# Kernel optimization log

Measured on AMD Instinct MI355X. Metric: run time of the kernel, lower is better.

## Reference

```python
import jax, jax.numpy as jnp
import numpy as np

NUM_HEADS = 16
EMB = 1024
HEAD = 64
SEQ = 2048
BATCH = 4


def setup_inputs() -> dict:
    key = jax.random.key(0)
    ks = jax.random.split(key, 6)
    s = EMB ** -0.5
    x = jax.random.normal(ks[0], (BATCH, SEQ, EMB), dtype=jnp.float32)
    # per-head projection weights stacked: [H, E, D] (Linear(emb, head, bias=False) per head)
    Wq = jax.random.normal(ks[1], (NUM_HEADS, EMB, HEAD), dtype=jnp.float32) * s
    Wk = jax.random.normal(ks[2], (NUM_HEADS, EMB, HEAD), dtype=jnp.float32) * s
    Wv = jax.random.normal(ks[3], (NUM_HEADS, EMB, HEAD), dtype=jnp.float32) * s
    # output projection Linear(head*num_heads, emb): weight [E, H*D], bias [E]
    Wo = jax.random.normal(ks[4], (EMB, NUM_HEADS * HEAD), dtype=jnp.float32) * ((NUM_HEADS * HEAD) ** -0.5)
    bo = jax.random.normal(ks[5], (EMB,), dtype=jnp.float32) * 0.01
    return {"x": x, "Wq": Wq, "Wk": Wk, "Wv": Wv, "Wo": Wo, "bo": bo}


def reference(x, Wq, Wk, Wv, Wo, bo):
    B, S, E = x.shape
    scale = HEAD ** -0.5
    # batched per-head projections: [B, H, S, D]
    q = jnp.einsum('bse,hed->bhsd', x, Wq)
    k = jnp.einsum('bse,hed->bhsd', x, Wk)
    v = jnp.einsum('bse,hed->bhsd', x, Wv)
    scores = jnp.einsum('bhqd,bhkd->bhqk', q, k) * scale
    causal = jnp.tril(jnp.ones((S, S), dtype=bool))
    scores = jnp.where(causal, scores, jnp.finfo(scores.dtype).min)
    attn = jax.nn.softmax(scores, axis=-1)  # dropout disabled (eval/deterministic)
    ctx = jnp.einsum('bhqk,bhkd->bhqd', attn, v)
    # concat heads along last dim (head-major order, matching torch.cat)
    concat = ctx.transpose(0, 2, 1, 3).reshape(B, S, NUM_HEADS * HEAD)
    out = concat @ Wo.T + bo
    return out
```

## Files before the change

kernel.cpp:

```cpp
#include <hip/hip_runtime.h>

#define NHEADS 16
#define EMB 1024
#define HDIM 64
#define SEQ 2048
#define BATCH 4

typedef unsigned short u16;
typedef __attribute__((ext_vector_type(8))) __bf16 bf16x8;
typedef __attribute__((ext_vector_type(4))) float f32x4;

#if __has_builtin(__builtin_amdgcn_exp2f)
#define EXP2(x) __builtin_amdgcn_exp2f(x)
#else
#define EXP2(x) __expf((x)*0.69314718056f)
#endif
#define CL2E 0.18033688011112042f

#define BARRIER() __builtin_amdgcn_s_barrier()
#define SB0() __builtin_amdgcn_sched_barrier(0)
#define PRIO1() __builtin_amdgcn_s_setprio(1)
#define PRIO0() __builtin_amdgcn_s_setprio(0)
#define VMCNT(n) asm volatile("s_waitcnt vmcnt(" #n ")" ::: "memory")

__device__ __forceinline__ u16 f2bf(float f) {
  union { float f; unsigned u; } v; v.f = f;
  unsigned r = v.u + 0x7fffu + ((v.u >> 16) & 1u);
  return (u16)(r >> 16);
}
__device__ __forceinline__ unsigned pk2bf(float a, float b) {
  union { __bf16 h[2]; unsigned u; } x;
  x.h[0] = (__bf16)a; x.h[1] = (__bf16)b; return x.u;
}
__device__ __forceinline__ void gl16(const void* g, void* l) {
  __builtin_amdgcn_global_load_lds(
      (const __attribute__((address_space(1))) unsigned*)g,
      (__attribute__((address_space(3))) unsigned*)l, 16, 0, 0);
}
__device__ __forceinline__ unsigned PKLO(unsigned a, unsigned b) {
  return __builtin_amdgcn_perm(a, b, 0x01000504u);
}
__device__ __forceinline__ unsigned PKHI(unsigned a, unsigned b) {
  return __builtin_amdgcn_perm(a, b, 0x03020706u);
}

__global__ __launch_bounds__(256) void k_cvt(const float* __restrict__ in,
                                             u16* __restrict__ out, int n4) {
  int i = blockIdx.x * 256 + threadIdx.x;
  if (i >= n4) return;
  f32x4 v = *(const f32x4*)(in + (size_t)i * 4);
  uint2 o;
  o.x = (unsigned)f2bf(v[0]) | ((unsigned)f2bf(v[1]) << 16);
  o.y = (unsigned)f2bf(v[2]) | ((unsigned)f2bf(v[3]) << 16);
  *(uint2*)(out + (size_t)i * 4) = o;
}

__global__ __launch_bounds__(256) void k_packw(const float* __restrict__ Wq,
                                               const float* __restrict__ Wk,
                                               const float* __restrict__ Wv,
                                               u16* __restrict__ Wt) {
  const int mh = blockIdx.x;
  const int e0 = blockIdx.y * 64;
  const int mtx = mh >> 4, h = mh & 15;
  const float* W = (mtx == 0 ? Wq : (mtx == 1 ? Wk : Wv)) + (size_t)h * EMB * HDIM;
  __shared__ u16 sT[64][65];
  const int t = threadIdx.x;
  {
    int e = t >> 2, d0 = (t & 3) * 16;
#pragma unroll
    for (int jj = 0; jj < 4; jj++) {
      f32x4 v = *(const f32x4*)(W + (size_t)(e0 + e) * HDIM + d0 + jj * 4);
#pragma unroll
      for (int kk = 0; kk < 4; kk++) sT[e][d0 + jj * 4 + kk] = f2bf(v[kk]);
    }
  }
  __syncthreads();
  {
    int d = t >> 2, eb = (t & 3) * 16;
#pragma unroll
    for (int j = 0; j < 16; j++)
      Wt[(size_t)(mh * 64 + d) * EMB + e0 + eb + j] = sT[eb + j][d];
  }
}

__global__ __launch_bounds__(512, 2) void k_gemm_qkv8(const u16* __restrict__ Xb,
                                                      const u16* __restrict__ Wt,
                                                      u16* __restrict__ Q,
                                                      u16* __restrict__ K,
                                                      u16* __restrict__ V) {
  extern __shared__ __align__(16) char smem[];
  const int bid = blockIdx.x;
  const int l = (bid & 7) * 64 + (bid >> 3);
  const int mt = l & 31, nt = l >> 5;
  const int m0 = mt * 256, n0 = nt * 192;

  const int t = threadIdx.x;
  const int wave = t >> 6, lane = t & 63, lr = lane & 15, lg = lane >> 4;
  const int wr = (wave >> 2) * 128;
  const int wc = (wave & 3) * 48;

  const f32x4 fz = {0.f, 0.f, 0.f, 0.f};
  f32x4 acc[8][3];
#pragma unroll
  for (int i = 0; i < 8; i++)
#pragma unroll
    for (int j = 0; j < 3; j++) acc[i][j] = fz;

  bf16x8 af[4][2], bfr[3][2];

  auto SROUND = [&](char* ldsbase, int rbase, const u16* src, int gRowBase, int kt) {
    int rs = rbase + wave * 8;
    int row = rs + (lane >> 3);
    int gc = (lane & 7) ^ (row & 7);
    gl16(src + (size_t)(gRowBase + row) * EMB + kt * 64 + gc * 8, ldsbase + rs * 128);
  };
  auto LOADA = [&](const char* bA, int mh) {
#pragma unroll
    for (int mf = 0; mf < 4; mf++)
#pragma unroll
      for (int kf = 0; kf < 2; kf++) {
        int row = wr + mh * 64 + mf * 16 + lr;
        af[mf][kf] = *(const bf16x8*)(bA + row * 128 + ((kf * 64 + lg * 16) ^ ((row & 7) << 4)));
      }
  };
  auto LOADB = [&](const char* bB) {
#pragma unroll
    for (int nf = 0; nf < 3; nf++)
#pragma unroll
      for (int kf = 0; kf < 2; kf++) {
        int row = wc + nf * 16 + lr;
        bfr[nf][kf] = *(const bf16x8*)(bB + row * 128 + ((kf * 64 + lg * 16) ^ ((row & 7) << 4)));
      }
  };

#define MFMAPH(MH)                                                                         \
  do {                                                                                     \
    _Pragma("unroll") for (int kf = 0; kf < 2; kf++)                                       \
    _Pragma("unroll") for (int mf = 0; mf < 4; mf++)                                       \
    _Pragma("unroll") for (int nf = 0; nf < 3; nf++)                                       \
      acc[(MH)*4 + mf][nf] = __builtin_amdgcn_mfma_f32_16x16x32_bf16(                      \
          af[mf][kf], bfr[nf][kf], acc[(MH)*4 + mf][nf], 0, 0, 0);                         \
  } while (0)

  const int NT = EMB / 64;
  {
    char* nA = smem;
    char* nB = smem + 32768;
    SROUND(nB, 0, Wt, n0, 0); SROUND(nB, 64, Wt, n0, 0); SROUND(nB, 128, Wt, n0, 0);
    SROUND(nA, 0, Xb, m0, 0);
    SROUND(nA, 64, Xb, m0, 0); SROUND(nA, 128, Xb, m0, 0); SROUND(nA, 192, Xb, m0, 0);
  }
  VMCNT(0);
  BARRIER();

  for (int tt = 0; tt < NT - 1; tt++) {
    const int cb = tt & 1, nb = cb ^ 1;
    char* bA = smem + cb * 57344;
    char* bB = bA + 32768;
    char* nA = smem + nb * 57344;
    char* nB = nA + 32768;
    SROUND(nB, 0, Wt, n0, tt + 1);
    SROUND(nB, 64, Wt, n0, tt + 1);
    SROUND(nB, 128, Wt, n0, tt + 1);
    SROUND(nA, 0, Xb, m0, tt + 1);
    VMCNT(5);
    BARRIER(); SB0();
    LOADA(bA, 0);
    LOADB(bB);
    PRIO1(); MFMAPH(0); PRIO0();
    BARRIER();
    SROUND(nA, 64, Xb, m0, tt + 1);
    SROUND(nA, 128, Xb, m0, tt + 1);
    SROUND(nA, 192, Xb, m0, tt + 1);
    VMCNT(7);
    BARRIER(); SB0();
    LOADA(bA, 1);
    PRIO1(); MFMAPH(1); PRIO0();
    BARRIER();
  }
  {
    char* bA = smem + ((NT - 1) & 1) * 57344;
    char* bB = bA + 32768;
    VMCNT(0);
    BARRIER(); SB0();
    LOADA(bA, 0);
    LOADB(bB);
    PRIO1(); MFMAPH(0); PRIO0();
    LOADA(bA, 1);
    PRIO1(); MFMAPH(1); PRIO0();
  }
#undef MFMAPH

  const int b = m0 >> 11;
  const int s0 = m0 & 2047;
#pragma unroll
  for (int am = 0; am < 8; am++)
#pragma unroll
    for (int nf = 0; nf < 3; nf++)
#pragma unroll
      for (int r = 0; r < 4; r++) {
        int row = wr + am * 16 + lg * 4 + r;
        int n = n0 + wc + nf * 16 + lr;
        int mtx = n >> 10, h = (n >> 6) & 15, d = n & 63;
        u16* dst = (mtx == 0 ? Q : (mtx == 1 ? K : V));
        dst[((size_t)(b * NHEADS + h) * SEQ + s0 + row) * HDIM + d] = f2bf(acc[am][nf][r]);
      }
}

__global__ __launch_bounds__(256, 3) void k_attn(const u16* __restrict__ Q,
                                                 const u16* __restrict__ K,
                                                 const u16* __restrict__ V,
                                                 u16* __restrict__ Cc) {
  const int bh = blockIdx.x;
  const int qt = 15 - (int)blockIdx.y;
  const int b = bh >> 4, h = bh & 15;
  const int t = threadIdx.x;
  const int wq = t >> 6, lane = t & 63, lr = lane & 15, lg = lane >> 4;
  const size_t base = (size_t)bh * SEQ * HDIM;

  __shared__ __align__(16) char sK[64 * 128];
  __shared__ __align__(16) char sV[64 * 128];
  __shared__ __align__(16) char sP[128 * 128];

#pragma unroll
  for (int i = 0; i < 4; i++) {
    int rb = wq * 32 + i * 8;
    int row = rb + (lane >> 3);
    int gc = (lane & 7) ^ (row & 7);
    gl16(Q + base + (size_t)(qt * 128 + row) * HDIM + gc * 8, sP + rb * 128);
  }
  __syncthreads();
  bf16x8 qf[2][2];
#pragma unroll
  for (int q2 = 0; q2 < 2; q2++)
#pragma unroll
    for (int kf = 0; kf < 2; kf++) {
      int row = wq * 32 + q2 * 16 + lr;
      qf[q2][kf] = *(const bf16x8*)(sP + row * 128 + ((kf * 64 + lg * 16) ^ ((row & 7) << 4)));
    }

  const f32x4 fz = {0.f, 0.f, 0.f, 0.f};
  f32x4 ot[4][2];
#pragma unroll
  for (int df = 0; df < 4; df++)
#pragma unroll
    for (int q2 = 0; q2 < 2; q2++) ot[df][q2] = fz;
  float m_[2] = {-1e30f, -1e30f}, l_[2] = {0.f, 0.f};

  const int nsteps = 2 * qt + 2;
  for (int step = 0; step < nsteps; step++) {
    const int k0 = step * 64;
    __syncthreads();
#pragma unroll
    for (int i = 0; i < 2; i++) {
      int rb = wq * 16 + i * 8;
      int row = rb + (lane >> 3);
      int gc = (lane & 7) ^ (row & 7);
      gl16(K + base + (size_t)(k0 + row) * HDIM + gc * 8, sK + rb * 128);
    }
    {
      const int kvb = (t & 15) * 4, db = (t >> 4) * 4;
      const u16* vp = V + base + (size_t)(k0 + kvb) * HDIM + db;
      uint2 v0 = *(const uint2*)(vp);
      uint2 v1 = *(const uint2*)(vp + HDIM);
      uint2 v2 = *(const uint2*)(vp + 2 * HDIM);
      uint2 v3 = *(const uint2*)(vp + 3 * HDIM);
      uint2 w0 = {PKLO(v0.x, v1.x), PKLO(v2.x, v3.x)};
      uint2 w1 = {PKHI(v0.x, v1.x), PKHI(v2.x, v3.x)};
      uint2 w2 = {PKLO(v0.y, v1.y), PKLO(v2.y, v3.y)};
      uint2 w3 = {PKHI(v0.y, v1.y), PKHI(v2.y, v3.y)};
      *(uint2*)(sV + (db + 0) * 128 + ((kvb * 2) ^ (((db + 0) & 7) << 4))) = w0;
      *(uint2*)(sV + (db + 1) * 128 + ((kvb * 2) ^ (((db + 1) & 7) << 4))) = w1;
      *(uint2*)(sV + (db + 2) * 128 + ((kvb * 2) ^ (((db + 2) & 7) << 4))) = w2;
      *(uint2*)(sV + (db + 3) * 128 + ((kvb * 2) ^ (((db + 3) & 7) << 4))) = w3;
    }
    __syncthreads();

    f32x4 st[4][2];
#pragma unroll
    for (int kvf = 0; kvf < 4; kvf++)
#pragma unroll
      for (int q2 = 0; q2 < 2; q2++) st[kvf][q2] = fz;
#pragma unroll
    for (int kf = 0; kf < 2; kf++) {
      bf16x8 kfr[4];
#pragma unroll
      for (int kvf = 0; kvf < 4; kvf++) {
        int row = kvf * 16 + lr;
        kfr[kvf] = *(const bf16x8*)(sK + row * 128 + ((kf * 64 + lg * 16) ^ ((row & 7) << 4)));
      }
#pragma unroll
      for (int kvf = 0; kvf < 4; kvf++)
#pragma unroll
        for (int q2 = 0; q2 < 2; q2++)
          st[kvf][q2] = __builtin_amdgcn_mfma_f32_16x16x32_bf16(kfr[kvf], qf[q2][kf], st[kvf][q2], 0, 0, 0);
    }

    const bool diag = (k0 >= qt * 128);
    float mxv[2];
#pragma unroll
    for (int q2 = 0; q2 < 2; q2++) {
      if (diag) {
        const int qg = qt * 128 + wq * 32 + q2 * 16 + lr;
#pragma unroll
        for (int kvf = 0; kvf < 4; kvf++)
#pragma unroll
          for (int r = 0; r < 4; r++)
            if (k0 + kvf * 16 + 4 * lg + r > qg) st[kvf][q2][r] = -3e38f;
      }
      float mx = -3e38f;
#pragma unroll
      for (int kvf = 0; kvf < 4; kvf++)
        mx = fmaxf(mx, fmaxf(fmaxf(st[kvf][q2][0], st[kvf][q2][1]),
                             fmaxf(st[kvf][q2][2], st[kvf][q2][3])));
      mx = fmaxf(mx, __shfl_xor(mx, 16));
      mx = fmaxf(mx, __shfl_xor(mx, 32));
      mxv[q2] = mx;
    }
    if (!__all((mxv[0] <= m_[0] + 64.f) && (mxv[1] <= m_[1] + 64.f))) {
#pragma unroll
      for (int q2 = 0; q2 < 2; q2++) {
        float mnew = fmaxf(m_[q2], mxv[q2]);
        float alpha = EXP2((m_[q2] - mnew) * CL2E);
        m_[q2] = mnew;
        l_[q2] *= alpha;
#pragma unroll
        for (int df = 0; df < 4; df++) ot[df][q2] *= alpha;
      }
    }
#pragma unroll
    for (int q2 = 0; q2 < 2; q2++) {
      float nmc = -m_[q2] * CL2E;
      float rs = 0.f;
      const int prow = wq * 32 + q2 * 16 + lr;
#pragma unroll
      for (int kvf = 0; kvf < 4; kvf++) {
        float p0 = EXP2(fmaf(st[kvf][q2][0], CL2E, nmc));
        float p1 = EXP2(fmaf(st[kvf][q2][1], CL2E, nmc));
        float p2 = EXP2(fmaf(st[kvf][q2][2], CL2E, nmc));
        float p3 = EXP2(fmaf(st[kvf][q2][3], CL2E, nmc));
        rs += (p0 + p1) + (p2 + p3);
        uint2 w;
        w.x = pk2bf(p0, p1);
        w.y = pk2bf(p2, p3);
        *(uint2*)(sP + prow * 128 + ((kvf * 32 + lg * 8) ^ ((prow & 7) << 4))) = w;
      }
      rs += __shfl_xor(rs, 16);
      rs += __shfl_xor(rs, 32);
      l_[q2] += rs;
    }

#pragma unroll
    for (int kf = 0; kf < 2; kf++) {
      bf16x8 pf[2], vf[4];
#pragma unroll
      for (int q2 = 0; q2 < 2; q2++) {
        int row = wq * 32 + q2 * 16 + lr;
        pf[q2] = *(const bf16x8*)(sP + row * 128 + ((kf * 64 + lg * 16) ^ ((row & 7) << 4)));
      }
#pragma unroll
      for (int df = 0; df < 4; df++) {
        int row = df * 16 + lr;
        vf[df] = *(const bf16x8*)(sV + row * 128 + ((kf * 64 + lg * 16) ^ ((row & 7) << 4)));
      }
#pragma unroll
      for (int df = 0; df < 4; df++)
#pragma unroll
        for (int q2 = 0; q2 < 2; q2++)
          ot[df][q2] = __builtin_amdgcn_mfma_f32_16x16x32_bf16(vf[df], pf[q2], ot[df][q2], 0, 0, 0);
    }
  }

#pragma unroll
  for (int q2 = 0; q2 < 2; q2++) {
    float inv = 1.0f / l_[q2];
    int s = qt * 128 + wq * 32 + q2 * 16 + lr;
#pragma unroll
    for (int df = 0; df < 4; df++) {
      uint2 w;
      w.x = pk2bf(ot[df][q2][0] * inv, ot[df][q2][1] * inv);
      w.y = pk2bf(ot[df][q2][2] * inv, ot[df][q2][3] * inv);
      *(uint2*)(Cc + ((size_t)b * SEQ + s) * (NHEADS * HDIM) + h * HDIM + df * 16 + 4 * lg) = w;
    }
  }
}

__global__ __launch_bounds__(256) void k_gemm_out(const u16* __restrict__ Cc,
                                                  const u16* __restrict__ Wob,
                                                  const float* __restrict__ bo,
                                                  float* __restrict__ out) {
  const int m0 = blockIdx.x * 128;
  const int n0 = blockIdx.y * 128;
  const int t = threadIdx.x;
  const int wave = t >> 6, lane = t & 63, lr = lane & 15, lg = lane >> 4;
  const int wr = (wave >> 1) * 64, wc = (wave & 1) * 64;

  __shared__ __align__(16) char sA[128 * 128];
  __shared__ __align__(16) char sB[128 * 128];

  const f32x4 fz = {0.f, 0.f, 0.f, 0.f};
  f32x4 acc[4][4];
#pragma unroll
  for (int i = 0; i < 4; i++)
#pragma unroll
    for (int j = 0; j < 4; j++) acc[i][j] = fz;

  for (int k0 = 0; k0 < EMB; k0 += 64) {
#pragma unroll
    for (int i = 0; i < 4; i++) {
      int rb = wave * 32 + i * 8;
      int row = rb + (lane >> 3);
      int gc = (lane & 7) ^ (row & 7);
      gl16(Cc + (size_t)(m0 + row) * EMB + k0 + gc * 8, sA + rb * 128);
      gl16(Wob + (size_t)(n0 + row) * EMB + k0 + gc * 8, sB + rb * 128);
    }
    __syncthreads();
    bf16x8 af[4][2], bfr[4][2];
#pragma unroll
    for (int mf = 0; mf < 4; mf++)
#pragma unroll
      for (int kf = 0; kf < 2; kf++) {
        int row = wr + mf * 16 + lr;
        af[mf][kf] = *(const bf16x8*)(sA + row * 128 + ((kf * 64 + lg * 16) ^ ((row & 7) << 4)));
      }
#pragma unroll
    for (int nf = 0; nf < 4; nf++)
#pragma unroll
      for (int kf = 0; kf < 2; kf++) {
        int row = wc + nf * 16 + lr;
        bfr[nf][kf] = *(const bf16x8*)(sB + row * 128 + ((kf * 64 + lg * 16) ^ ((row & 7) << 4)));
      }
#pragma unroll
    for (int kf = 0; kf < 2; kf++)
#pragma unroll
      for (int mf = 0; mf < 4; mf++)
#pragma unroll
        for (int nf = 0; nf < 4; nf++)
          acc[mf][nf] = __builtin_amdgcn_mfma_f32_16x16x32_bf16(af[mf][kf], bfr[nf][kf], acc[mf][nf], 0, 0, 0);
    __syncthreads();
  }

  float bv[4];
#pragma unroll
  for (int nf = 0; nf < 4; nf++) bv[nf] = bo[n0 + wc + nf * 16 + lr];
#pragma unroll
  for (int mf = 0; mf < 4; mf++)
#pragma unroll
    for (int nf = 0; nf < 4; nf++)
#pragma unroll
      for (int r = 0; r < 4; r++) {
        int row = wr + mf * 16 + lg * 4 + r;
        int n = n0 + wc + nf * 16 + lr;
        out[(size_t)(m0 + row) * EMB + n] = acc[mf][nf][r] + bv[nf];
      }
}

extern "C" void kernel_launch(void* const* d_in, const int* in_sizes, int n_in,
                              void* d_out, int out_size, void* d_ws, size_t ws_size,
                              hipStream_t stream) {
  const float* x  = (const float*)d_in[0];
  const float* Wq = (const float*)d_in[1];
  const float* Wk = (const float*)d_in[2];
  const float* Wv = (const float*)d_in[3];
  const float* Wo = (const float*)d_in[4];
  const float* bo = (const float*)d_in[5];
  float* out = (float*)d_out;

  char* ws = (char*)d_ws;
  const size_t SZ_XB  = (size_t)8192 * 1024 * 2;
  const size_t SZ_WT  = (size_t)3072 * 1024 * 2;
  const size_t SZ_WOB = (size_t)1024 * 1024 * 2;
  const size_t SZ_QKV = (size_t)64 * 2048 * 64 * 2;
  u16* Xb  = (u16*)(ws);
  u16* Wt  = (u16*)(ws + SZ_XB);
  u16* Wob = (u16*)(ws + SZ_XB + SZ_WT);
  u16* Qb  = (u16*)(ws + SZ_XB + SZ_WT + SZ_WOB);
  u16* Kb  = (u16*)(ws + SZ_XB + SZ_WT + SZ_WOB + SZ_QKV);
  u16* Vb  = (u16*)(ws + SZ_XB + SZ_WT + SZ_WOB + 2 * SZ_QKV);
  u16* Cc  = (u16*)(ws + SZ_XB + SZ_WT + SZ_WOB + 3 * SZ_QKV);

  k_cvt<<<8192, 256, 0, stream>>>(x, Xb, 2097152);
  k_cvt<<<1024, 256, 0, stream>>>(Wo, Wob, 262144);
  k_packw<<<dim3(48, 16), 256, 0, stream>>>(Wq, Wk, Wv, Wt);
  k_gemm_qkv8<<<512, 512, 114688, stream>>>(Xb, Wt, Qb, Kb, Vb);
  k_attn<<<dim3(64, 16), 256, 0, stream>>>(Qb, Kb, Vb, Cc);
  k_gemm_out<<<dim3(64, 8), 256, 0, stream>>>(Cc, Wob, bo, out);
}
```

Before: 172.3 us.

## Double-buffer K/V tiles in attention to prefetch next tile during compute

The attention kernel now keeps two LDS buffers each for K and V. It issues the global loads for the next K/V tile before the QK^T and PV math on the current tile, and writes the transposed V into the alternate buffer afterwards. This replaces the two block-wide syncs per step with a single barrier at the end of each step, aiming to hide global-load latency behind MFMA work. In exchange, LDS use per block grows from 32 KB to 48 KB, and the V prefetch registers stay live across the compute, which may pressure occupancy at 3 blocks per CU.

```diff
diff --git a/kernel.cpp b/kernel.cpp
--- a/kernel.cpp
+++ b/kernel.cpp
@@ -22,6 +22,7 @@
 #define PRIO1() __builtin_amdgcn_s_setprio(1)
 #define PRIO0() __builtin_amdgcn_s_setprio(0)
 #define VMCNT(n) asm volatile("s_waitcnt vmcnt(" #n ")" ::: "memory")
+#define LGKM0() asm volatile("s_waitcnt lgkmcnt(0)" ::: "memory")
 
 __device__ __forceinline__ u16 f2bf(float f) {
   union { float f; unsigned u; } v; v.f = f;
@@ -218,9 +219,38 @@
   const int wq = t >> 6, lane = t & 63, lr = lane & 15, lg = lane >> 4;
   const size_t base = (size_t)bh * SEQ * HDIM;
 
-  __shared__ __align__(16) char sK[64 * 128];
-  __shared__ __align__(16) char sV[64 * 128];
+  __shared__ __align__(16) char sK[2][64 * 128];
+  __shared__ __align__(16) char sV[2][64 * 128];
   __shared__ __align__(16) char sP[128 * 128];
+
+  const int kvb = (t & 15) * 4, db = (t >> 4) * 4;
+  uint2 v0, v1, v2, v3;
+  auto VLOAD = [&](int k0) {
+    const u16* vp = V + base + (size_t)(k0 + kvb) * HDIM + db;
+    v0 = *(const uint2*)(vp);
+    v1 = *(const uint2*)(vp + HDIM);
+    v2 = *(const uint2*)(vp + 2 * HDIM);
+    v3 = *(const uint2*)(vp + 3 * HDIM);
+  };
+  auto VWRITE = [&](char* sv) {
+    uint2 w0 = {PKLO(v0.x, v1.x), PKLO(v2.x, v3.x)};
+    uint2 w1 = {PKHI(v0.x, v1.x), PKHI(v2.x, v3.x)};
+    uint2 w2 = {PKLO(v0.y, v1.y), PKLO(v2.y, v3.y)};
+    uint2 w3 = {PKHI(v0.y, v1.y), PKHI(v2.y, v3.y)};
+    *(uint2*)(sv + (db + 0) * 128 + ((kvb * 2) ^ (((db + 0) & 7) << 4))) = w0;
+    *(uint2*)(sv + (db + 1) * 128 + ((kvb * 2) ^ (((db + 1) & 7) << 4))) = w1;
+    *(uint2*)(sv + (db + 2) * 128 + ((kvb * 2) ^ (((db + 2) & 7) << 4))) = w2;
+    *(uint2*)(sv + (db + 3) * 128 + ((kvb * 2) ^ (((db + 3) & 7) << 4))) = w3;
+  };
+  auto KSTAGE = [&](char* sk, int k0) {
+#pragma unroll
+    for (int i = 0; i < 2; i++) {
+      int rb = wq * 16 + i * 8;
+      int row = rb + (lane >> 3);
+      int gc = (lane & 7) ^ (row & 7);
+      gl16(K + base + (size_t)(k0 + row) * HDIM + gc * 8, sk + rb * 128);
+    }
+  };
 
 #pragma unroll
   for (int i = 0; i < 4; i++) {
@@ -229,7 +259,12 @@
     int gc = (lane & 7) ^ (row & 7);
     gl16(Q + base + (size_t)(qt * 128 + row) * HDIM + gc * 8, sP + rb * 128);
   }
+  KSTAGE(sK[0], 0);
+  VLOAD(0);
+  VMCNT(0);
+  VWRITE(sV[0]);
   __syncthreads();
+
   bf16x8 qf[2][2];
 #pragma unroll
   for (int q2 = 0; q2 < 2; q2++)
@@ -250,31 +285,12 @@
   const int nsteps = 2 * qt + 2;
   for (int step = 0; step < nsteps; step++) {
     const int k0 = step * 64;
-    __syncthreads();
-#pragma unroll
-    for (int i = 0; i < 2; i++) {
-      int rb = wq * 16 + i * 8;
-      int row = rb + (lane >> 3);
-      int gc = (lane & 7) ^ (row & 7);
-      gl16(K + base + (size_t)(k0 + row) * HDIM + gc * 8, sK + rb * 128);
-    }
-    {
-      const int kvb = (t & 15) * 4, db = (t >> 4) * 4;
-      const u16* vp = V + base + (size_t)(k0 + kvb) * HDIM + db;
-      uint2 v0 = *(const uint2*)(vp);
-      uint2 v1 = *(const uint2*)(vp + HDIM);
-      uint2 v2 = *(const uint2*)(vp + 2 * HDIM);
-      uint2 v3 = *(const uint2*)(vp + 3 * HDIM);
-      uint2 w0 = {PKLO(v0.x, v1.x), PKLO(v2.x, v3.x)};
-      uint2 w1 = {PKHI(v0.x, v1.x), PKHI(v2.x, v3.x)};
-      uint2 w2 = {PKLO(v0.y, v1.y), PKLO(v2.y, v3.y)};
-      uint2 w3 = {PKHI(v0.y, v1.y), PKHI(v2.y, v3.y)};
-      *(uint2*)(sV + (db + 0) * 128 + ((kvb * 2) ^ (((db + 0) & 7) << 4))) = w0;
-      *(uint2*)(sV + (db + 1) * 128 + ((kvb * 2) ^ (((db + 1) & 7) << 4))) = w1;
-      *(uint2*)(sV + (db + 2) * 128 + ((kvb * 2) ^ (((db + 2) & 7) << 4))) = w2;
-      *(uint2*)(sV + (db + 3) * 128 + ((kvb * 2) ^ (((db + 3) & 7) << 4))) = w3;
-    }
-    __syncthreads();
+    const int cur = step & 1, nxt = cur ^ 1;
+    const bool pf = (step + 1 < nsteps);
+    if (pf) {
+      KSTAGE(sK[nxt], k0 + 64);
+      VLOAD(k0 + 64);
+    }
 
     f32x4 st[4][2];
 #pragma unroll
@@ -287,7 +303,7 @@
 #pragma unroll
       for (int kvf = 0; kvf < 4; kvf++) {
         int row = kvf * 16 + lr;
-        kfr[kvf] = *(const bf16x8*)(sK + row * 128 + ((kf * 64 + lg * 16) ^ ((row & 7) << 4)));
+        kfr[kvf] = *(const bf16x8*)(sK[cur] + row * 128 + ((kf * 64 + lg * 16) ^ ((row & 7) << 4)));
       }
 #pragma unroll
       for (int kvf = 0; kvf < 4; kvf++)
@@ -352,22 +368,29 @@
 
 #pragma unroll
     for (int kf = 0; kf < 2; kf++) {
-      bf16x8 pf[2], vf[4];
+      bf16x8 pfg[2], vf[4];
 #pragma unroll
       for (int q2 = 0; q2 < 2; q2++) {
         int row = wq * 32 + q2 * 16 + lr;
-        pf[q2] = *(const bf16x8*)(sP + row * 128 + ((kf * 64 + lg * 16) ^ ((row & 7) << 4)));
+        pfg[q2] = *(const bf16x8*)(sP + row * 128 + ((kf * 64 + lg * 16) ^ ((row & 7) << 4)));
       }
 #pragma unroll
       for (int df = 0; df < 4; df++) {
         int row = df * 16 + lr;
-        vf[df] = *(const bf16x8*)(sV + row * 128 + ((kf * 64 + lg * 16) ^ ((row & 7) << 4)));
+        vf[df] = *(const bf16x8*)(sV[cur] + row * 128 + ((kf * 64 + lg * 16) ^ ((row & 7) << 4)));
       }
 #pragma unroll
       for (int df = 0; df < 4; df++)
 #pragma unroll
         for (int q2 = 0; q2 < 2; q2++)
-          ot[df][q2] = __builtin_amdgcn_mfma_f32_16x16x32_bf16(vf[df], pf[q2], ot[df][q2], 0, 0, 0);
+          ot[df][q2] = __builtin_amdgcn_mfma_f32_16x16x32_bf16(vf[df], pfg[q2], ot[df][q2], 0, 0, 0);
+    }
+
+    if (pf) {
+      VMCNT(0);
+      VWRITE(sV[nxt]);
+      LGKM0();
+      BARRIER();
     }
   }
 
```

Measured after the change: 164.9 us. 4.3% less time.
